# Kernel optimization log

Measured on AMD Instinct MI355X. Metric: run time of the kernel, lower is better.

The kernel has to match this reference:

```python
import jax, jax.numpy as jnp
import numpy as np

N = 32768   # atoms/nodes
E = 4       # chemical elements
C = 128     # input channels per irrep
K = 128     # output channels per irrep
LMAX = 3    # 4 l-blocks -> 16 lm rows


def setup_inputs() -> dict:
    key = jax.random.key(0)
    kx, ky, kw = jax.random.split(key, 3)
    x = jax.random.normal(kx, (N, (LMAX + 1) ** 2, C), dtype=jnp.float32)
    # one-hot element encoding per node
    elem = jax.random.randint(ky, (N,), 0, E)
    y = jax.nn.one_hot(elem, E, dtype=jnp.float32)
    # per-element, per-l weight blocks [E, 4, C, K]
    weights = jax.random.normal(kw, (E, LMAX + 1, C, K), dtype=jnp.float32)
    return {"x": x, "y": y, "weights": weights}


def reference(x, y, weights):
    # x: [N, 16, C]  y: [N, E] one-hot  weights: [E, 4, C, K]
    n, _, c = x.shape
    e, nl, _, k = weights.shape
    path_weight = 1.0 / jnp.sqrt(jnp.asarray(c, x.dtype))  # e3nn uvw normalization
    outs = []
    for l in range(nl):
        s = l * l
        m = 2 * l + 1
        xb = x[:, s:s + m, :]                      # [N, 2l+1, C]
        acc = jnp.zeros((n, m, k), x.dtype)
        for el in range(e):
            # mask-weighted grouped GEMM: only nodes of element `el` contribute
            acc = acc + y[:, el, None, None] * jnp.einsum('nmc,ck->nmk', xb, weights[el, l])
        outs.append(acc * path_weight)
    return jnp.concatenate(outs, axis=1)           # [N, 16, K]
```

## Files before the change

### kernel.cpp

```cpp
#include <hip/hip_runtime.h>

#define NS 32768
#define NE 4

typedef __attribute__((ext_vector_type(4))) float f32x4;
typedef __attribute__((ext_vector_type(8))) short bf16x8;

__device__ __forceinline__ unsigned short f2bf(float f) {
    unsigned int u = __float_as_uint(f);
    u = (u + 0x7fffu + ((u >> 16) & 1u)) >> 16;
    return (unsigned short)u;
}

__global__ void prep_kernel(const float* __restrict__ W,
                            unsigned short* __restrict__ Wt,
                            const float* __restrict__ y,
                            int* __restrict__ cnt, int* __restrict__ idx) {
    const int b = blockIdx.x;
    if (b < 16) {
        const float* w = W + (size_t)b * 16384;
        unsigned short* wt = Wt + (size_t)b * 16384;
        for (int i = threadIdx.x; i < 16384; i += 256) {
            int c = i & 127, k = i >> 7;
            wt[k * 128 + c] = f2bf(w[c * 128 + k]);
        }
        return;
    }
    int n = (b - 16) * 256 + threadIdx.x;
    const float4 yr = ((const float4*)y)[n];
    int e = 0;
    if (yr.y > 0.5f) e = 1;
    else if (yr.z > 0.5f) e = 2;
    else if (yr.w > 0.5f) e = 3;
    const int lane = threadIdx.x & 63;
    int pos = 0;
#pragma unroll
    for (int ee = 0; ee < NE; ++ee) {
        unsigned long long m = __ballot(e == ee);
        if (m == 0) continue;
        int leader = __builtin_ctzll(m);
        int base = 0;
        if (lane == leader) base = atomicAdd(&cnt[ee], __popcll(m));
        base = __shfl(base, leader);
        if (e == ee) pos = base + __popcll(m & ((1ull << lane) - 1ull));
    }
    idx[e * NS + pos] = n;
}

template <int L, int M>
__device__ __forceinline__ void gemm_body(
    int e, int bi, int nb, unsigned char* lds, const float* __restrict__ x,
    const unsigned short* __restrict__ Wt, const int* __restrict__ cnt,
    const int* __restrict__ idx, float* __restrict__ out) {
    const int rows_total = cnt[e] * M;

    {
        const unsigned char* wp =
            (const unsigned char*)(Wt + (size_t)(e * 4 + L) * 16384);
        const int t = threadIdx.x;
#pragma unroll
        for (int q = 0; q < 8; ++q) {
            int o = q * 4096 + t * 16;
            uint4 v = *(const uint4*)(wp + o);
            int so = o ^ (((o >> 8) & 7) << 4);
            *(uint4*)(lds + so) = v;
        }
    }
    __syncthreads();

    const int lane = threadIdx.x & 63;
    const int wv = threadIdx.x >> 6;
    const int li = lane & 15;
    const int half = lane >> 4;
    const int i5 = lane >> 5;
    const int c32 = lane & 31;
    unsigned char* xl = lds + 32768 + wv * 4096;

    for (int tile = bi; tile * 64 < rows_total; tile += nb) {
        int g = tile * 64 + wv * 16 + li;
        bool valid = g < rows_total;
        int gc = valid ? g : rows_total - 1;
        int pos = gc / M;
        int jj = gc - pos * M;
        int xrow = idx[e * NS + pos] * 16 + L * L + jj;

        f32x4 bv[8];
#pragma unroll
        for (int q = 0; q < 8; ++q) {
            int tr = 2 * q + i5;
            int nr = __shfl(xrow, tr);
            bv[q] = *(const f32x4*)(x + (size_t)nr * 128 + c32 * 4);
        }
#pragma unroll
        for (int q = 0; q < 8; ++q) {
            int tr = 2 * q + i5;
            unsigned int p0 = (unsigned int)f2bf(bv[q].x) |
                              ((unsigned int)f2bf(bv[q].y) << 16);
            unsigned int p1 = (unsigned int)f2bf(bv[q].z) |
                              ((unsigned int)f2bf(bv[q].w) << 16);
            uint2 pk; pk.x = p0; pk.y = p1;
            int off = (c32 * 8) ^ ((tr & 7) << 4);
            *(uint2*)(xl + tr * 256 + off) = pk;
        }

        f32x4 acc[8];
#pragma unroll
        for (int t = 0; t < 8; ++t) acc[t] = (f32x4){0.f, 0.f, 0.f, 0.f};

#pragma unroll
        for (int kk = 0; kk < 4; ++kk) {
            int co = (kk * 64 + half * 16) ^ ((li & 7) << 4);
            bf16x8 bfrag = *(const bf16x8*)(xl + li * 256 + co);
#pragma unroll
            for (int t = 0; t < 8; ++t) {
                bf16x8 afrag = *(const bf16x8*)(lds + (t * 16 + li) * 256 + co);
                acc[t] = __builtin_amdgcn_mfma_f32_16x16x32_bf16(afrag, bfrag,
                                                                 acc[t], 0, 0, 0);
            }
        }

        if (valid) {
            float* orow = out + (size_t)xrow * 128;
            const float pw = 0.088388347648318447f;
#pragma unroll
            for (int t = 0; t < 8; ++t) {
                *(f32x4*)(orow + t * 16 + half * 4) = acc[t] * pw;
            }
        }
    }
}

__global__ __launch_bounds__(256, 3) void gemm_main(
    const float* __restrict__ x, const unsigned short* __restrict__ Wt,
    const int* __restrict__ cnt, const int* __restrict__ idx,
    float* __restrict__ out) {
    __shared__ __align__(16) unsigned char lds[49152];
    const int b = blockIdx.x;
    const int e = b >> 9;
    const int r = b & 511;
    if (r < 32)       gemm_body<0, 1>(e, r,       32,  lds, x, Wt, cnt, idx, out);
    else if (r < 128) gemm_body<1, 3>(e, r - 32,  96,  lds, x, Wt, cnt, idx, out);
    else if (r < 288) gemm_body<2, 5>(e, r - 128, 160, lds, x, Wt, cnt, idx, out);
    else              gemm_body<3, 7>(e, r - 288, 224, lds, x, Wt, cnt, idx, out);
}

extern "C" void kernel_launch(void* const* d_in, const int* in_sizes, int n_in,
                              void* d_out, int out_size, void* d_ws,
                              size_t ws_size, hipStream_t stream) {
    const float* x = (const float*)d_in[0];
    const float* y = (const float*)d_in[1];
    const float* W = (const float*)d_in[2];
    float* out = (float*)d_out;

    char* ws = (char*)d_ws;
    int* cnt = (int*)ws;
    int* idx = (int*)(ws + 64);
    unsigned short* Wt = (unsigned short*)(ws + 64 + NE * NS * 4);

    hipMemsetAsync(cnt, 0, NE * sizeof(int), stream);
    prep_kernel<<<16 + NS / 256, 256, 0, stream>>>(W, Wt, y, cnt, idx);
    gemm_main<<<2048, 256, 0, stream>>>(x, Wt, cnt, idx, out);
}
```

Baseline: 158.2 us.

## Double-buffer x tile loads in registers and shrink grid to persistent size

The gather loads of x for the next tile are now issued before the current tile's convert, MFMA and store work, using two alternating register buffers. This is meant to hide global-load latency in a memory-bound grouped GEMM. The grid also drops from 2048 to 768 blocks, with each element and l-block share scaled down, so each block loops over more tiles. The extra 32 floats of prefetch registers per thread could raise register pressure under the existing launch bounds.

```diff
diff --git a/kernel.cpp b/kernel.cpp
--- a/kernel.cpp
+++ b/kernel.cpp
@@ -48,6 +48,66 @@
 }
 
 template <int L, int M>
+__device__ __forceinline__ void load_tile(
+    const float* __restrict__ x, const int* __restrict__ idx, int e,
+    int rows_total, int tile, int wv, int li, int i5, int c32,
+    int& xrow, bool& valid, f32x4* bv) {
+    int g = tile * 64 + wv * 16 + li;
+    valid = g < rows_total;
+    int gc = valid ? g : rows_total - 1;
+    int pos = gc / M;
+    int jj = gc - pos * M;
+    xrow = idx[e * NS + pos] * 16 + L * L + jj;
+#pragma unroll
+    for (int q = 0; q < 8; ++q) {
+        int nr = __shfl(xrow, 2 * q + i5);
+        bv[q] = *(const f32x4*)(x + (size_t)nr * 128 + c32 * 4);
+    }
+}
+
+__device__ __forceinline__ void compute_tile(
+    unsigned char* __restrict__ lds, unsigned char* __restrict__ xl,
+    const f32x4* bv, int xrow, bool valid, int li, int half, int i5, int c32,
+    float* __restrict__ out) {
+#pragma unroll
+    for (int q = 0; q < 8; ++q) {
+        int tr = 2 * q + i5;
+        unsigned int p0 = (unsigned int)f2bf(bv[q].x) |
+                          ((unsigned int)f2bf(bv[q].y) << 16);
+        unsigned int p1 = (unsigned int)f2bf(bv[q].z) |
+                          ((unsigned int)f2bf(bv[q].w) << 16);
+        uint2 pk; pk.x = p0; pk.y = p1;
+        int off = (c32 * 8) ^ ((tr & 7) << 4);
+        *(uint2*)(xl + tr * 256 + off) = pk;
+    }
+
+    f32x4 acc[8];
+#pragma unroll
+    for (int t = 0; t < 8; ++t) acc[t] = (f32x4){0.f, 0.f, 0.f, 0.f};
+
+#pragma unroll
+    for (int kk = 0; kk < 4; ++kk) {
+        int co = (kk * 64 + half * 16) ^ ((li & 7) << 4);
+        bf16x8 bfrag = *(const bf16x8*)(xl + li * 256 + co);
+#pragma unroll
+        for (int t = 0; t < 8; ++t) {
+            bf16x8 afrag = *(const bf16x8*)(lds + (t * 16 + li) * 256 + co);
+            acc[t] = __builtin_amdgcn_mfma_f32_16x16x32_bf16(afrag, bfrag,
+                                                             acc[t], 0, 0, 0);
+        }
+    }
+
+    if (valid) {
+        float* orow = out + (size_t)xrow * 128;
+        const float pw = 0.088388347648318447f;
+#pragma unroll
+        for (int t = 0; t < 8; ++t) {
+            *(f32x4*)(orow + t * 16 + half * 4) = acc[t] * pw;
+        }
+    }
+}
+
+template <int L, int M>
 __device__ __forceinline__ void gemm_body(
     int e, int bi, int nb, unsigned char* lds, const float* __restrict__ x,
     const unsigned short* __restrict__ Wt, const int* __restrict__ cnt,
@@ -76,57 +136,31 @@
     const int c32 = lane & 31;
     unsigned char* xl = lds + 32768 + wv * 4096;
 
-    for (int tile = bi; tile * 64 < rows_total; tile += nb) {
-        int g = tile * 64 + wv * 16 + li;
-        bool valid = g < rows_total;
-        int gc = valid ? g : rows_total - 1;
-        int pos = gc / M;
-        int jj = gc - pos * M;
-        int xrow = idx[e * NS + pos] * 16 + L * L + jj;
+    int tile = bi;
+    if (tile * 64 >= rows_total) return;
 
-        f32x4 bv[8];
-#pragma unroll
-        for (int q = 0; q < 8; ++q) {
-            int tr = 2 * q + i5;
-            int nr = __shfl(xrow, tr);
-            bv[q] = *(const f32x4*)(x + (size_t)nr * 128 + c32 * 4);
-        }
-#pragma unroll
-        for (int q = 0; q < 8; ++q) {
-            int tr = 2 * q + i5;
-            unsigned int p0 = (unsigned int)f2bf(bv[q].x) |
-                              ((unsigned int)f2bf(bv[q].y) << 16);
-            unsigned int p1 = (unsigned int)f2bf(bv[q].z) |
-                              ((unsigned int)f2bf(bv[q].w) << 16);
-            uint2 pk; pk.x = p0; pk.y = p1;
-            int off = (c32 * 8) ^ ((tr & 7) << 4);
-            *(uint2*)(xl + tr * 256 + off) = pk;
-        }
+    int xrowA, xrowB;
+    bool vA, vB;
+    f32x4 bvA[8], bvB[8];
 
-        f32x4 acc[8];
-#pragma unroll
-        for (int t = 0; t < 8; ++t) acc[t] = (f32x4){0.f, 0.f, 0.f, 0.f};
-
-#pragma unroll
-        for (int kk = 0; kk < 4; ++kk) {
-            int co = (kk * 64 + half * 16) ^ ((li & 7) << 4);
-            bf16x8 bfrag = *(const bf16x8*)(xl + li * 256 + co);
-#pragma unroll
-            for (int t = 0; t < 8; ++t) {
-                bf16x8 afrag = *(const bf16x8*)(lds + (t * 16 + li) * 256 + co);
-                acc[t] = __builtin_amdgcn_mfma_f32_16x16x32_bf16(afrag, bfrag,
-                                                                 acc[t], 0, 0, 0);
-            }
-        }
-
-        if (valid) {
-            float* orow = out + (size_t)xrow * 128;
-            const float pw = 0.088388347648318447f;
-#pragma unroll
-            for (int t = 0; t < 8; ++t) {
-                *(f32x4*)(orow + t * 16 + half * 4) = acc[t] * pw;
-            }
-        }
+    load_tile<L, M>(x, idx, e, rows_total, tile, wv, li, i5, c32, xrowA, vA, bvA);
+    for (;;) {
+        int tn = tile + nb;
+        bool hn = (tn * 64 < rows_total);
+        if (hn)
+            load_tile<L, M>(x, idx, e, rows_total, tn, wv, li, i5, c32, xrowB,
+                            vB, bvB);
+        compute_tile(lds, xl, bvA, xrowA, vA, li, half, i5, c32, out);
+        if (!hn) break;
+        tile = tn;
+        tn += nb;
+        hn = (tn * 64 < rows_total);
+        if (hn)
+            load_tile<L, M>(x, idx, e, rows_total, tn, wv, li, i5, c32, xrowA,
+                            vA, bvA);
+        compute_tile(lds, xl, bvB, xrowB, vB, li, half, i5, c32, out);
+        if (!hn) break;
+        tile = tn;
     }
 }
 
@@ -136,12 +170,12 @@
     float* __restrict__ out) {
     __shared__ __align__(16) unsigned char lds[49152];
     const int b = blockIdx.x;
-    const int e = b >> 9;
-    const int r = b & 511;
-    if (r < 32)       gemm_body<0, 1>(e, r,       32,  lds, x, Wt, cnt, idx, out);
-    else if (r < 128) gemm_body<1, 3>(e, r - 32,  96,  lds, x, Wt, cnt, idx, out);
-    else if (r < 288) gemm_body<2, 5>(e, r - 128, 160, lds, x, Wt, cnt, idx, out);
-    else              gemm_body<3, 7>(e, r - 288, 224, lds, x, Wt, cnt, idx, out);
+    const int e = b / 192;
+    const int r = b % 192;
+    if (r < 12)       gemm_body<0, 1>(e, r,       12, lds, x, Wt, cnt, idx, out);
+    else if (r < 48)  gemm_body<1, 3>(e, r - 12,  36, lds, x, Wt, cnt, idx, out);
+    else if (r < 108) gemm_body<2, 5>(e, r - 48,  60, lds, x, Wt, cnt, idx, out);
+    else              gemm_body<3, 7>(e, r - 108, 84, lds, x, Wt, cnt, idx, out);
 }
 
 extern "C" void kernel_launch(void* const* d_in, const int* in_sizes, int n_in,
@@ -159,5 +193,5 @@
 
     hipMemsetAsync(cnt, 0, NE * sizeof(int), stream);
     prep_kernel<<<16 + NS / 256, 256, 0, stream>>>(W, Wt, y, cnt, idx);
-    gemm_main<<<2048, 256, 0, stream>>>(x, Wt, cnt, idx, out);
+    gemm_main<<<768, 256, 0, stream>>>(x, Wt, cnt, idx, out);
 }
```

New measurement: 320.0 us. 102% more time.

## Replace atomic node bucketing with count-scan-fill for deterministic ordered indices

Applied to the files above, without the earlier changes.

Node-to-element bucketing is split into three kernels: per-block counts, a single-block prefix scan, and a fill pass that writes each node at a rank computed without contended global atomics. Within each element the index list is now in ascending node order instead of atomic arrival order. That ordering should give the GEMM's gathered x rows and scattered output rows more locality. The cost is two extra kernel launches and a second read of y.

```diff
diff --git a/kernel.cpp b/kernel.cpp
--- a/kernel.cpp
+++ b/kernel.cpp
@@ -12,10 +12,18 @@
     return (unsigned short)u;
 }
 
-__global__ void prep_kernel(const float* __restrict__ W,
-                            unsigned short* __restrict__ Wt,
-                            const float* __restrict__ y,
-                            int* __restrict__ cnt, int* __restrict__ idx) {
+__device__ __forceinline__ int expert_of(const float4 yr) {
+    int e = 0;
+    if (yr.y > 0.5f) e = 1;
+    else if (yr.z > 0.5f) e = 2;
+    else if (yr.w > 0.5f) e = 3;
+    return e;
+}
+
+__global__ void prep_count(const float* __restrict__ W,
+                           unsigned short* __restrict__ Wt,
+                           const float* __restrict__ y,
+                           int* __restrict__ bcnt) {
     const int b = blockIdx.x;
     if (b < 16) {
         const float* w = W + (size_t)b * 16384;
@@ -26,25 +34,55 @@
         }
         return;
     }
-    int n = (b - 16) * 256 + threadIdx.x;
-    const float4 yr = ((const float4*)y)[n];
-    int e = 0;
-    if (yr.y > 0.5f) e = 1;
-    else if (yr.z > 0.5f) e = 2;
-    else if (yr.w > 0.5f) e = 3;
+    const int blk = b - 16;
+    int n = blk * 256 + threadIdx.x;
+    int e = expert_of(((const float4*)y)[n]);
     const int lane = threadIdx.x & 63;
-    int pos = 0;
 #pragma unroll
     for (int ee = 0; ee < NE; ++ee) {
         unsigned long long m = __ballot(e == ee);
-        if (m == 0) continue;
-        int leader = __builtin_ctzll(m);
-        int base = 0;
-        if (lane == leader) base = atomicAdd(&cnt[ee], __popcll(m));
-        base = __shfl(base, leader);
-        if (e == ee) pos = base + __popcll(m & ((1ull << lane) - 1ull));
-    }
-    idx[e * NS + pos] = n;
+        if (lane == 0 && m) atomicAdd(&bcnt[ee * 128 + blk], __popcll(m));
+    }
+}
+
+__global__ void prep_scan(const int* __restrict__ bcnt, int* __restrict__ boff,
+                          int* __restrict__ cnt) {
+    __shared__ int s[512];
+    const int t = threadIdx.x;
+    int v = bcnt[t];
+    s[t] = v;
+    __syncthreads();
+    for (int d = 1; d < 512; d <<= 1) {
+        int add = (t >= d) ? s[t - d] : 0;
+        __syncthreads();
+        s[t] += add;
+        __syncthreads();
+    }
+    int seg = (t >= 128) ? s[(t >> 7) * 128 - 1] : 0;
+    boff[t] = s[t] - v - seg;
+    if ((t & 127) == 127) cnt[t >> 7] = s[t] - seg;
+}
+
+__global__ void prep_fill(const float* __restrict__ y,
+                          const int* __restrict__ boff, int* __restrict__ idx) {
+    __shared__ int wcnt[4][4];
+    const int blk = blockIdx.x;
+    int n = blk * 256 + threadIdx.x;
+    int e = expert_of(((const float4*)y)[n]);
+    const int lane = threadIdx.x & 63;
+    const int wv = threadIdx.x >> 6;
+    int rank = 0;
+#pragma unroll
+    for (int ee = 0; ee < NE; ++ee) {
+        unsigned long long m = __ballot(e == ee);
+        if (lane == 0) wcnt[wv][ee] = __popcll(m);
+        if (e == ee) rank = __popcll(m & ((1ull << lane) - 1ull));
+    }
+    __syncthreads();
+#pragma unroll
+    for (int w = 0; w < 4; ++w)
+        if (w < wv) rank += wcnt[w][e];
+    idx[e * NS + boff[e * 128 + blk] + rank] = n;
 }
 
 template <int L, int M>
@@ -156,8 +194,12 @@
     int* cnt = (int*)ws;
     int* idx = (int*)(ws + 64);
     unsigned short* Wt = (unsigned short*)(ws + 64 + NE * NS * 4);
-
-    hipMemsetAsync(cnt, 0, NE * sizeof(int), stream);
-    prep_kernel<<<16 + NS / 256, 256, 0, stream>>>(W, Wt, y, cnt, idx);
+    int* bcnt = (int*)(ws + 64 + NE * NS * 4 + 16 * 16384 * 2);
+    int* boff = bcnt + 512;
+
+    hipMemsetAsync(bcnt, 0, 512 * sizeof(int), stream);
+    prep_count<<<16 + 128, 256, 0, stream>>>(W, Wt, y, bcnt);
+    prep_scan<<<1, 512, 0, stream>>>(bcnt, boff, cnt);
+    prep_fill<<<128, 256, 0, stream>>>(y, boff, idx);
     gemm_main<<<2048, 256, 0, stream>>>(x, Wt, cnt, idx, out);
 }
```

Measured after the change: 142.6 us. 9.8% less time.
